# Kernel optimization log

Hardware: AMD Instinct MI355X
Metric: run time of the kernel (lower is better)

## Reference

```python
import jax, jax.numpy as jnp
import numpy as np

N_NODES = 50000

def _graph_conv(x, src, dst, W, b, n):
    # DGL GraphConv, norm='both': D_dst^{-1/2} * sum_edges(D_src^{-1/2} * (x W)) + b
    xw = x @ W  # [N, out]
    ones = jnp.ones(src.shape, jnp.float32)
    deg_out = jnp.maximum(jax.ops.segment_sum(ones, src, num_segments=n), 1.0)
    deg_in = jnp.maximum(jax.ops.segment_sum(ones, dst, num_segments=n), 1.0)
    norm_src = deg_out ** -0.5
    norm_dst = deg_in ** -0.5
    msg = xw[src] * norm_src[src][:, None]          # [E, out] gather
    agg = jax.ops.segment_sum(msg, dst, num_segments=n)  # [N, out] scatter-add
    return agg * norm_dst[:, None] + b


def _rgcn_layer(x, src, dst, W, b, n):
    # HeteroGraphConv with aggregate='sum' over relations
    out = _graph_conv(x, src[0], dst[0], W[0], b[0], n)
    for r in range(1, src.shape[0]):
        out = out + _graph_conv(x, src[r], dst[r], W[r], b[r], n)
    return out


def setup_inputs() -> dict:
    key = jax.random.key(0)
    ks = jax.random.split(key, 9)
    R, E = 3, 200000
    din, dhid, dout = 128, 128, 64
    x = jax.random.normal(ks[0], (N_NODES, din), jnp.float32)
    src = jax.random.randint(ks[1], (R, E), 0, N_NODES, jnp.int32)
    dst = jax.random.randint(ks[2], (R, E), 0, N_NODES, jnp.int32)
    neg_src = jax.random.randint(ks[3], (E,), 0, N_NODES, jnp.int32)
    neg_dst = jax.random.randint(ks[4], (E,), 0, N_NODES, jnp.int32)
    W1 = jax.random.normal(ks[5], (R, din, dhid), jnp.float32) / np.sqrt(din)
    b1 = jnp.zeros((R, dhid), jnp.float32)
    W2 = jax.random.normal(ks[6], (R, dhid, dout), jnp.float32) / np.sqrt(dhid)
    b2 = jnp.zeros((R, dout), jnp.float32)
    return {"x": x, "src": src, "dst": dst, "neg_src": neg_src,
            "neg_dst": neg_dst, "W1": W1, "b1": b1, "W2": W2, "b2": b2}


def reference(x, src, dst, neg_src, neg_dst, W1, b1, W2, b2):
    n = x.shape[0]
    h = jax.nn.relu(_rgcn_layer(x, src, dst, W1, b1, n))
    h = _rgcn_layer(h, src, dst, W2, b2, n)  # [N, out]
    # HeteroDotProductPredictor on etype = relation 0 (u_dot_v -> [E, 1])
    pos = jnp.sum(h[src[0]] * h[dst[0]], axis=-1, keepdims=True)
    neg = jnp.sum(h[neg_src] * h[neg_dst], axis=-1, keepdims=True)
    return pos, neg
```

## Files before the change

### kernel.cpp

```cpp
#include <hip/hip_runtime.h>

#define N_NODES 50000
#define E_EDGES 200000
#define R_REL 3
#define D_IN 128
#define D_HID 128
#define D_OUT 64
#define N_SCAN (R_REL * N_NODES)
#define BCAP 16
#define OVCAP 4096

typedef __attribute__((ext_vector_type(8))) short bf16x8;
typedef __attribute__((ext_vector_type(4))) float f32x4;

__device__ inline unsigned short f2bf(float v) {
    union { float f; unsigned int u; } x; x.f = v;
    unsigned int r = x.u + 0x7fffu + ((x.u >> 16) & 1u);
    return (unsigned short)(r >> 16);
}
__device__ inline float bf2f(unsigned short h) {
    union { unsigned int u; float f; } x; x.u = ((unsigned int)h) << 16; return x.f;
}
__device__ inline float bf_lo(unsigned int p) {
    union { unsigned int u; float f; } x; x.u = p << 16; return x.f;
}
__device__ inline float bf_hi(unsigned int p) {
    union { unsigned int u; float f; } x; x.u = p & 0xffff0000u; return x.f;
}

__global__ __launch_bounds__(256) void k_zero_i32(int* __restrict__ p, int n) {
    int i = blockIdx.x * 256 + threadIdx.x;
    if (i < n) p[i] = 0;
}

__global__ __launch_bounds__(256) void k_count_prep(const int* __restrict__ src,
                                                    const int* __restrict__ dst,
                                                    const float* __restrict__ x,
                                                    const float* __restrict__ W1,
                                                    const float* __restrict__ W2,
                                                    const float* __restrict__ b1,
                                                    int* __restrict__ deg_out,
                                                    int* __restrict__ cnt_in,
                                                    int* __restrict__ ov_cnt,
                                                    uint2* __restrict__ ovlist,
                                                    int* __restrict__ bucket,
                                                    unsigned int* __restrict__ xb,
                                                    unsigned short* __restrict__ w1t_h,
                                                    unsigned short* __restrict__ w1t_l,
                                                    unsigned short* __restrict__ w2t_h,
                                                    unsigned short* __restrict__ w2t_l,
                                                    float* __restrict__ bsum) {
    int i = blockIdx.x * 256 + threadIdx.x;
    if (i < 400000) {
#pragma unroll
        for (int k = 0; k < 4; k++) {
            int q = i * 4 + k;
            float4 v = ((const float4*)x)[q];
            uint2 u;
            u.x = ((unsigned int)f2bf(v.y) << 16) | f2bf(v.x);
            u.y = ((unsigned int)f2bf(v.w) << 16) | f2bf(v.z);
            ((uint2*)xb)[q] = u;
        }
    }
    if (i < R_REL * D_IN * D_HID) {
        int r = i >> 14;
        int kk = (i >> 7) & 127;
        int c = i & 127;
        float v = W1[i];
        unsigned short h = f2bf(v);
        unsigned short l = f2bf(v - bf2f(h));
        int o = r * 16384 + c * 128 + kk;
        w1t_h[o] = h;
        w1t_l[o] = l;
    }
    if (i < R_REL * D_HID * D_OUT) {
        int r = i >> 13;
        int kk = (i >> 6) & 127;
        int cl = i & 63;
        float v = W2[i];
        unsigned short h = f2bf(v);
        unsigned short l = f2bf(v - bf2f(h));
        int o = (r * 64 + cl) * 128 + kk;
        w2t_h[o] = h;
        w2t_l[o] = l;
    }
    if (i < 128) bsum[i] = b1[i] + b1[128 + i] + b1[256 + i];
    if (i < R_REL * E_EDGES) {
        int r = i / E_EDGES;
        int s = src[i];
        int d = dst[i];
        atomicAdd(&deg_out[r * N_NODES + s], 1);
        int bin = r * N_NODES + d;
        int pos = atomicAdd(&cnt_in[bin], 1);
        if (pos < BCAP) {
            bucket[bin * BCAP + pos] = s;
        } else {
            int oi = atomicAdd(ov_cnt, 1);
            if (oi < OVCAP) {
                uint2 e;
                e.x = (unsigned int)bin;
                e.y = (unsigned int)s;
                ovlist[oi] = e;
            }
        }
    }
}

__global__ __launch_bounds__(256) void k_rednorm(const int* __restrict__ deg_out,
                                                 const int* __restrict__ cnt_in,
                                                 float* __restrict__ norm_out,
                                                 float* __restrict__ norm_in) {
    int b = blockIdx.x * 256 + threadIdx.x;
    if (b >= N_SCAN) return;
    int o = deg_out[b];
    int d = cnt_in[b];
    norm_out[b] = rsqrtf((float)(o > 1 ? o : 1));
    norm_in[b] = rsqrtf((float)(d > 1 ? d : 1));
}

__global__ __launch_bounds__(256) void k_agg128(const int* __restrict__ cnt_r,
                                                const int* __restrict__ bucket_r,
                                                const float* __restrict__ nout_r,
                                                const float* __restrict__ nin_r,
                                                const int* __restrict__ ov_cnt,
                                                const uint2* __restrict__ ovlist,
                                                int rbase,
                                                const unsigned int* __restrict__ xb,
                                                float* __restrict__ agg) {
    int w = (blockIdx.x * 256 + threadIdx.x) >> 6;
    if (w >= N_NODES) return;
    int lane = threadIdx.x & 63;
    const unsigned int* tab = xb + lane;
    int n = cnt_r[w];
    int nn = n < BCAP ? n : BCAP;
    float ax = 0.f, ay = 0.f;
    int j = 0;
    for (; j + 4 <= nn; j += 4) {
        uint4 s4 = *(const uint4*)&bucket_r[w * BCAP + j];
        float c0 = nout_r[s4.x], c1 = nout_r[s4.y];
        float c2 = nout_r[s4.z], c3 = nout_r[s4.w];
        unsigned int p0 = tab[s4.x * 64], p1 = tab[s4.y * 64];
        unsigned int p2 = tab[s4.z * 64], p3 = tab[s4.w * 64];
        ax += c0 * bf_lo(p0); ay += c0 * bf_hi(p0);
        ax += c1 * bf_lo(p1); ay += c1 * bf_hi(p1);
        ax += c2 * bf_lo(p2); ay += c2 * bf_hi(p2);
        ax += c3 * bf_lo(p3); ay += c3 * bf_hi(p3);
    }
    for (; j < nn; j++) {
        unsigned int s = (unsigned int)bucket_r[w * BCAP + j];
        float c = nout_r[s];
        unsigned int p = tab[s * 64];
        ax += c * bf_lo(p);
        ay += c * bf_hi(p);
    }
    int oc = *ov_cnt;
    if (oc > 0) {
        if (oc > OVCAP) oc = OVCAP;
        for (int k = 0; k < oc; k++) {
            uint2 e = ovlist[k];
            if ((int)e.x == rbase + w) {
                float c = nout_r[e.y];
                unsigned int p = tab[e.y * 64];
                ax += c * bf_lo(p);
                ay += c * bf_hi(p);
            }
        }
    }
    float ni = nin_r[w];
    float2 o;
    o.x = ax * ni;
    o.y = ay * ni;
    *(float2*)&agg[w * 128 + lane * 2] = o;
}

template <int MODE>
__global__ __launch_bounds__(256) void k_mm1(const float* __restrict__ A,
                                             const unsigned short* __restrict__ wt_h,
                                             const unsigned short* __restrict__ wt_l,
                                             const float* __restrict__ bsum,
                                             float* __restrict__ h1f,
                                             unsigned short* __restrict__ h1h,
                                             unsigned short* __restrict__ h1l,
                                             int M) {
    __shared__ short sAh[2048], sAl[2048];
    __shared__ short sWh[4096], sWl[4096];
    int t = threadIdx.x;
    int row0 = blockIdx.x * 64;
    int wid = t >> 6;
    int lane = t & 63;
    int lr = lane & 15;
    int lkg = lane >> 4;
    int wr = (wid & 1) * 32;
    int wc = (wid >> 1) * 64;

    f32x4 acc[2][4];
#pragma unroll
    for (int i = 0; i < 2; i++)
#pragma unroll
        for (int j = 0; j < 4; j++) acc[i][j] = (f32x4)(0.f);

    int arow = t >> 2;
    int akg = t & 3;

    for (int k0 = 0; k0 < 128; k0 += 32) {
        {
            int gr = row0 + arow;
            float v[8];
            if (gr < M) {
                float4 p0 = *(const float4*)&A[gr * 128 + k0 + akg * 8];
                float4 p1 = *(const float4*)&A[gr * 128 + k0 + akg * 8 + 4];
                v[0] = p0.x; v[1] = p0.y; v[2] = p0.z; v[3] = p0.w;
                v[4] = p1.x; v[5] = p1.y; v[6] = p1.z; v[7] = p1.w;
            } else {
#pragma unroll
                for (int e = 0; e < 8; e++) v[e] = 0.f;
            }
            short hh[8], ll[8];
#pragma unroll
            for (int e = 0; e < 8; e++) {
                unsigned short h = f2bf(v[e]);
                hh[e] = (short)h;
                ll[e] = (short)f2bf(v[e] - bf2f(h));
            }
            int cidx = akg * 64 + arow;
            *(bf16x8*)&sAh[cidx * 8] = *(bf16x8*)hh;
            *(bf16x8*)&sAl[cidx * 8] = *(bf16x8*)ll;
        }
#pragma unroll
        for (int itr = 0; itr < 2; itr++) {
            int cc = t + itr * 256;
            int col = cc >> 2;
            int kg = cc & 3;
            int go = col * 128 + k0 + kg * 8;
            int cidx = kg * 128 + col;
            *(bf16x8*)&sWh[cidx * 8] = *(const bf16x8*)&wt_h[go];
            *(bf16x8*)&sWl[cidx * 8] = *(const bf16x8*)&wt_l[go];
        }
        __syncthreads();
        bf16x8 ah[2], al[2], bh[4], bl[4];
#pragma unroll
        for (int i = 0; i < 2; i++) {
            int cidx = lkg * 64 + wr + i * 16 + lr;
            ah[i] = *(const bf16x8*)&sAh[cidx * 8];
            al[i] = *(const bf16x8*)&sAl[cidx * 8];
        }
#pragma unroll
        for (int j = 0; j < 4; j++) {
            int cidx = lkg * 128 + wc + j * 16 + lr;
            bh[j] = *(const bf16x8*)&sWh[cidx * 8];
            bl[j] = *(const bf16x8*)&sWl[cidx * 8];
        }
#pragma unroll
        for (int i = 0; i < 2; i++)
#pragma unroll
            for (int j = 0; j < 4; j++) {
                acc[i][j] = __builtin_amdgcn_mfma_f32_16x16x32_bf16(ah[i], bh[j], acc[i][j], 0, 0, 0);
                acc[i][j] = __builtin_amdgcn_mfma_f32_16x16x32_bf16(ah[i], bl[j], acc[i][j], 0, 0, 0);
                acc[i][j] = __builtin_amdgcn_mfma_f32_16x16x32_bf16(al[i], bh[j], acc[i][j], 0, 0, 0);
            }
        __syncthreads();
    }
#pragma unroll
    for (int i = 0; i < 2; i++)
#pragma unroll
        for (int q = 0; q < 4; q++) {
            int gr = row0 + wr + i * 16 + lkg * 4 + q;
            if (gr >= M) continue;
#pragma unroll
            for (int j = 0; j < 4; j++) {
                int gc = wc + j * 16 + lr;
                float v = acc[i][j][q];
                if (MODE == 0) {
                    h1f[gr * 128 + gc] = v + bsum[gc];
                } else if (MODE == 1) {
                    h1f[gr * 128 + gc] += v;
                } else {
                    float u = fmaxf(h1f[gr * 128 + gc] + v, 0.f);
                    unsigned short h = f2bf(u);
                    h1h[gr * 128 + gc] = h;
                    h1l[gr * 128 + gc] = f2bf(u - bf2f(h));
                }
            }
        }
}

__global__ __launch_bounds__(256) void k_mm2(const unsigned short* __restrict__ h1h,
                                             const unsigned short* __restrict__ h1l,
                                             const unsigned short* __restrict__ wt_h,
                                             const unsigned short* __restrict__ wt_l,
                                             const float* __restrict__ norm_out,
                                             unsigned short* __restrict__ xwb2, int M) {
    __shared__ short sAh[2048], sAl[2048];
    __shared__ short sWh[6144], sWl[6144];
    int t = threadIdx.x;
    int row0 = blockIdx.x * 64;
    int wid = t >> 6;
    int lane = t & 63;
    int lr = lane & 15;
    int lkg = lane >> 4;
    int wr = (wid & 1) * 32;
    int wc = (wid >> 1) * 96;

    f32x4 acc[2][6];
#pragma unroll
    for (int i = 0; i < 2; i++)
#pragma unroll
        for (int j = 0; j < 6; j++) acc[i][j] = (f32x4)(0.f);

    int arow = t >> 2;
    int akg = t & 3;

    for (int k0 = 0; k0 < 128; k0 += 32) {
        {
            int gr = row0 + arow;
            int cidx = akg * 64 + arow;
            if (gr < M) {
                int go = gr * 128 + k0 + akg * 8;
                *(bf16x8*)&sAh[cidx * 8] = *(const bf16x8*)&h1h[go];
                *(bf16x8*)&sAl[cidx * 8] = *(const bf16x8*)&h1l[go];
            } else {
                *(bf16x8*)&sAh[cidx * 8] = (bf16x8)(short)0;
                *(bf16x8*)&sAl[cidx * 8] = (bf16x8)(short)0;
            }
        }
#pragma unroll
        for (int itr = 0; itr < 3; itr++) {
            int cc = t + itr * 256;
            int col = cc >> 2;
            int kg = cc & 3;
            int go = col * 128 + k0 + kg * 8;
            int cidx = kg * 192 + col;
            *(bf16x8*)&sWh[cidx * 8] = *(const bf16x8*)&wt_h[go];
            *(bf16x8*)&sWl[cidx * 8] = *(const bf16x8*)&wt_l[go];
        }
        __syncthreads();
        bf16x8 ah[2], al[2];
#pragma unroll
        for (int i = 0; i < 2; i++) {
            int cidx = lkg * 64 + wr + i * 16 + lr;
            ah[i] = *(const bf16x8*)&sAh[cidx * 8];
            al[i] = *(const bf16x8*)&sAl[cidx * 8];
        }
#pragma unroll
        for (int j = 0; j < 6; j++) {
            int cidx = lkg * 192 + wc + j * 16 + lr;
            bf16x8 bh = *(const bf16x8*)&sWh[cidx * 8];
            bf16x8 bl = *(const bf16x8*)&sWl[cidx * 8];
#pragma unroll
            for (int i = 0; i < 2; i++) {
                acc[i][j] = __builtin_amdgcn_mfma_f32_16x16x32_bf16(ah[i], bh, acc[i][j], 0, 0, 0);
                acc[i][j] = __builtin_amdgcn_mfma_f32_16x16x32_bf16(ah[i], bl, acc[i][j], 0, 0, 0);
                acc[i][j] = __builtin_amdgcn_mfma_f32_16x16x32_bf16(al[i], bh, acc[i][j], 0, 0, 0);
            }
        }
        __syncthreads();
    }
#pragma unroll
    for (int i = 0; i < 2; i++)
#pragma unroll
        for (int q = 0; q < 4; q++) {
            int gr = row0 + wr + i * 16 + lkg * 4 + q;
            if (gr >= M) continue;
#pragma unroll
            for (int j = 0; j < 6; j++) {
                int gc = wc + j * 16 + lr;
                float sc = norm_out[(gc >> 6) * N_NODES + gr];
                xwb2[gr * 192 + gc] = f2bf(acc[i][j][q] * sc);
            }
        }
}

__global__ __launch_bounds__(256) void k_agg64f(const int* __restrict__ cnt_in,
                                                const int* __restrict__ bucket,
                                                const float* __restrict__ norm_in,
                                                const int* __restrict__ ov_cnt,
                                                const uint2* __restrict__ ovlist,
                                                const unsigned short* __restrict__ xwb,
                                                const float* __restrict__ b2,
                                                unsigned short* __restrict__ h2b) {
    int w = (blockIdx.x * 256 + threadIdx.x) >> 6;
    if (w >= N_NODES) return;
    int lane = threadIdx.x & 63;
    float acc = b2[lane] + b2[64 + lane] + b2[128 + lane];
    int oc = *ov_cnt;
    if (oc > OVCAP) oc = OVCAP;
#pragma unroll
    for (int r = 0; r < R_REL; r++) {
        const unsigned short* tab = xwb + r * 64 + lane;
        int bin = r * N_NODES + w;
        int n = cnt_in[bin];
        int nn = n < BCAP ? n : BCAP;
        float a = 0.f;
        int j = 0;
        for (; j + 4 <= nn; j += 4) {
            uint4 s4 = *(const uint4*)&bucket[bin * BCAP + j];
            float v0 = bf2f(tab[s4.x * 192]);
            float v1 = bf2f(tab[s4.y * 192]);
            float v2 = bf2f(tab[s4.z * 192]);
            float v3 = bf2f(tab[s4.w * 192]);
            a += v0 + v1 + v2 + v3;
        }
        for (; j < nn; j++) {
            unsigned int s = (unsigned int)bucket[bin * BCAP + j];
            a += bf2f(tab[s * 192]);
        }
        if (oc > 0) {
            for (int k = 0; k < oc; k++) {
                uint2 e = ovlist[k];
                if ((int)e.x == bin) a += bf2f(tab[e.y * 192]);
            }
        }
        acc += norm_in[bin] * a;
    }
    h2b[w * 64 + lane] = f2bf(acc);
}

__global__ __launch_bounds__(256) void k_predict(const int* __restrict__ sa,
                                                 const int* __restrict__ sb,
                                                 const int* __restrict__ na,
                                                 const int* __restrict__ nb,
                                                 const unsigned short* __restrict__ h2b,
                                                 float* __restrict__ out) {
    int tid = blockIdx.x * 256 + threadIdx.x;
    int p = tid >> 4;
    if (p >= 2 * E_EDGES) return;
    int lane = tid & 15;
    int ia, ib;
    if (p < E_EDGES) { ia = sa[p]; ib = sb[p]; }
    else             { ia = na[p - E_EDGES]; ib = nb[p - E_EDGES]; }
    uint2 ua = *(const uint2*)&h2b[ia * 64 + lane * 4];
    uint2 ub = *(const uint2*)&h2b[ib * 64 + lane * 4];
    float d = bf_lo(ua.x) * bf_lo(ub.x) + bf_hi(ua.x) * bf_hi(ub.x)
            + bf_lo(ua.y) * bf_lo(ub.y) + bf_hi(ua.y) * bf_hi(ub.y);
    d += __shfl_xor(d, 1);
    d += __shfl_xor(d, 2);
    d += __shfl_xor(d, 4);
    d += __shfl_xor(d, 8);
    if (lane == 0) out[p] = d;
}


extern "C" void kernel_launch(void* const* d_in, const int* in_sizes, int n_in,
                              void* d_out, int out_size, void* d_ws, size_t ws_size,
                              hipStream_t stream) {
    (void)in_sizes; (void)n_in; (void)out_size; (void)ws_size;
    const float* x       = (const float*)d_in[0];
    const int*   src     = (const int*)d_in[1];
    const int*   dst     = (const int*)d_in[2];
    const int*   neg_src = (const int*)d_in[3];
    const int*   neg_dst = (const int*)d_in[4];
    const float* W1      = (const float*)d_in[5];
    const float* b1      = (const float*)d_in[6];
    const float* W2      = (const float*)d_in[7];
    const float* b2      = (const float*)d_in[8];
    float* out = (float*)d_out;
    float* ws  = (float*)d_ws;

    float* norm_out = ws;
    float* norm_in  = ws + N_SCAN;
    int*   deg_out  = (int*)(ws + 300000);
    int*   cnt_in   = (int*)(ws + 450000);
    int*   ov_cnt   = (int*)(ws + 600000);
    uint2* ovlist   = (uint2*)(ws + 600016);
    int*   bucket   = (int*)(ws + 608208);
    unsigned short* w1t_h = (unsigned short*)(ws + 3008208);
    unsigned short* w1t_l = (unsigned short*)(ws + 3032784);
    unsigned short* w2t_h = (unsigned short*)(ws + 3057360);
    unsigned short* w2t_l = (unsigned short*)(ws + 3069648);
    float* bsum     = ws + 3081936;
    float* agg      = ws + 3082064;
    unsigned short* xwb2 = (unsigned short*)(ws + 3082064);
    float* h1f      = ws + 9482064;
    unsigned short* h2b  = (unsigned short*)(ws + 9482064);
    unsigned short* h1h  = (unsigned short*)(ws + 15882064);
    unsigned short* h1l  = (unsigned short*)(ws + 19082064);
    unsigned int*   xb   = (unsigned int*)(ws + 19082064);

    const int NB_CP   = (R_REL * E_EDGES + 255) / 256;
    const int NB_WAVE = (N_NODES * 64 + 255) / 256;
    const int NB_MM   = (N_NODES + 63) / 64;

    k_zero_i32<<<(300016 + 255) / 256, 256, 0, stream>>>(deg_out, 300016);
    k_count_prep<<<NB_CP, 256, 0, stream>>>(src, dst, x, W1, W2, b1,
                                            deg_out, cnt_in, ov_cnt, ovlist, bucket,
                                            xb, w1t_h, w1t_l, w2t_h, w2t_l, bsum);
    k_rednorm<<<(N_SCAN + 255) / 256, 256, 0, stream>>>(deg_out, cnt_in, norm_out, norm_in);

    for (int r = 0; r < R_REL; r++) {
        k_agg128<<<NB_WAVE, 256, 0, stream>>>(cnt_in + r * N_NODES,
                                              bucket + r * N_NODES * BCAP,
                                              norm_out + r * N_NODES,
                                              norm_in + r * N_NODES,
                                              ov_cnt, ovlist, r * N_NODES, xb, agg);
        if (r == 0)
            k_mm1<0><<<NB_MM, 256, 0, stream>>>(agg, w1t_h, w1t_l, bsum, h1f, h1h, h1l, N_NODES);
        else if (r == 1)
            k_mm1<1><<<NB_MM, 256, 0, stream>>>(agg, w1t_h + 16384, w1t_l + 16384, bsum, h1f, h1h, h1l, N_NODES);
        else
            k_mm1<2><<<NB_MM, 256, 0, stream>>>(agg, w1t_h + 32768, w1t_l + 32768, bsum, h1f, h1h, h1l, N_NODES);
    }

    k_mm2<<<NB_MM, 256, 0, stream>>>(h1h, h1l, w2t_h, w2t_l, norm_out, xwb2, N_NODES);
    k_agg64f<<<NB_WAVE, 256, 0, stream>>>(cnt_in, bucket, norm_in, ov_cnt, ovlist,
                                          xwb2, b2, h2b);

    k_predict<<<(2 * E_EDGES * 16 + 255) / 256, 256, 0, stream>>>(
        src, dst, neg_src, neg_dst, h2b, out);
}
```

Before: 272.2 us.

## Batch layer-1 aggregation across relations, store bf16, fuse into one K=384 GEMM

The three per-relation aggregate+GEMM launch pairs become one aggregation kernel over a 2D grid (node, relation) that writes normalized aggregates as bf16. A single GEMM then runs K=384 across the concatenated relation aggregates with bias and ReLU in the epilogue, so the fp32 h1 read-modify-write passes and the A-side hi/lo split are gone. This drops one of the three MFMAs per tile. The count_prep grid is also interleaved so edge-counting blocks and conversion blocks mix, and bucket indices are loaded as four uint4 into an unrolled predicated loop. The cost is lower precision: the aggregated activations lose their low bf16 part.

```diff
diff --git a/kernel.cpp b/kernel.cpp
--- a/kernel.cpp
+++ b/kernel.cpp
@@ -9,6 +9,8 @@
 #define N_SCAN (R_REL * N_NODES)
 #define BCAP 16
 #define OVCAP 4096
+#define NBE 2344
+#define NBP 1563
 
 typedef __attribute__((ext_vector_type(8))) short bf16x8;
 typedef __attribute__((ext_vector_type(4))) float f32x4;
@@ -50,42 +52,13 @@
                                                     unsigned short* __restrict__ w2t_h,
                                                     unsigned short* __restrict__ w2t_l,
                                                     float* __restrict__ bsum) {
-    int i = blockIdx.x * 256 + threadIdx.x;
-    if (i < 400000) {
-#pragma unroll
-        for (int k = 0; k < 4; k++) {
-            int q = i * 4 + k;
-            float4 v = ((const float4*)x)[q];
-            uint2 u;
-            u.x = ((unsigned int)f2bf(v.y) << 16) | f2bf(v.x);
-            u.y = ((unsigned int)f2bf(v.w) << 16) | f2bf(v.z);
-            ((uint2*)xb)[q] = u;
-        }
-    }
-    if (i < R_REL * D_IN * D_HID) {
-        int r = i >> 14;
-        int kk = (i >> 7) & 127;
-        int c = i & 127;
-        float v = W1[i];
-        unsigned short h = f2bf(v);
-        unsigned short l = f2bf(v - bf2f(h));
-        int o = r * 16384 + c * 128 + kk;
-        w1t_h[o] = h;
-        w1t_l[o] = l;
-    }
-    if (i < R_REL * D_HID * D_OUT) {
-        int r = i >> 13;
-        int kk = (i >> 6) & 127;
-        int cl = i & 63;
-        float v = W2[i];
-        unsigned short h = f2bf(v);
-        unsigned short l = f2bf(v - bf2f(h));
-        int o = (r * 64 + cl) * 128 + kk;
-        w2t_h[o] = h;
-        w2t_l[o] = l;
-    }
-    if (i < 128) bsum[i] = b1[i] + b1[128 + i] + b1[256 + i];
-    if (i < R_REL * E_EDGES) {
+    int g = blockIdx.x / 5;
+    int m = blockIdx.x % 5;
+    int t = threadIdx.x;
+    if (m < 3) {
+        int eb = g * 3 + m;
+        int i = eb * 256 + t;
+        if (i >= R_REL * E_EDGES) return;
         int r = i / E_EDGES;
         int s = src[i];
         int d = dst[i];
@@ -103,6 +76,43 @@
                 ovlist[oi] = e;
             }
         }
+    } else {
+        int pb = g * 2 + (m - 3);
+        int i = pb * 256 + t;
+        if (i < 400000) {
+#pragma unroll
+            for (int k = 0; k < 4; k++) {
+                int q = i * 4 + k;
+                float4 v = ((const float4*)x)[q];
+                uint2 u;
+                u.x = ((unsigned int)f2bf(v.y) << 16) | f2bf(v.x);
+                u.y = ((unsigned int)f2bf(v.w) << 16) | f2bf(v.z);
+                ((uint2*)xb)[q] = u;
+            }
+        }
+        if (i < R_REL * D_IN * D_HID) {
+            int r = i >> 14;
+            int kk = (i >> 7) & 127;
+            int c = i & 127;
+            float v = W1[i];
+            unsigned short h = f2bf(v);
+            unsigned short l = f2bf(v - bf2f(h));
+            int o = r * 16384 + c * 128 + kk;
+            w1t_h[o] = h;
+            w1t_l[o] = l;
+        }
+        if (i < R_REL * D_HID * D_OUT) {
+            int r = i >> 13;
+            int kk = (i >> 6) & 127;
+            int cl = i & 63;
+            float v = W2[i];
+            unsigned short h = f2bf(v);
+            unsigned short l = f2bf(v - bf2f(h));
+            int o = (r * 64 + cl) * 128 + kk;
+            w2t_h[o] = h;
+            w2t_l[o] = l;
+        }
+        if (i < 128) bsum[i] = b1[i] + b1[128 + i] + b1[256 + i];
     }
 }
 
@@ -118,71 +128,64 @@
     norm_in[b] = rsqrtf((float)(d > 1 ? d : 1));
 }
 
-__global__ __launch_bounds__(256) void k_agg128(const int* __restrict__ cnt_r,
-                                                const int* __restrict__ bucket_r,
-                                                const float* __restrict__ nout_r,
-                                                const float* __restrict__ nin_r,
+__global__ __launch_bounds__(256) void k_aggall(const int* __restrict__ cnt_in,
+                                                const int* __restrict__ bucket,
+                                                const float* __restrict__ norm_out,
+                                                const float* __restrict__ norm_in,
                                                 const int* __restrict__ ov_cnt,
                                                 const uint2* __restrict__ ovlist,
-                                                int rbase,
                                                 const unsigned int* __restrict__ xb,
-                                                float* __restrict__ agg) {
+                                                unsigned int* __restrict__ aggh) {
     int w = (blockIdx.x * 256 + threadIdx.x) >> 6;
     if (w >= N_NODES) return;
+    int r = blockIdx.y;
     int lane = threadIdx.x & 63;
     const unsigned int* tab = xb + lane;
-    int n = cnt_r[w];
+    const float* nout = norm_out + r * N_NODES;
+    int bin = r * N_NODES + w;
+    int n = cnt_in[bin];
+    const uint4* bp = (const uint4*)(bucket + bin * BCAP);
+    uint4 q0 = bp[0], q1 = bp[1], q2 = bp[2], q3 = bp[3];
+    unsigned int sl[16] = {q0.x, q0.y, q0.z, q0.w, q1.x, q1.y, q1.z, q1.w,
+                           q2.x, q2.y, q2.z, q2.w, q3.x, q3.y, q3.z, q3.w};
     int nn = n < BCAP ? n : BCAP;
     float ax = 0.f, ay = 0.f;
-    int j = 0;
-    for (; j + 4 <= nn; j += 4) {
-        uint4 s4 = *(const uint4*)&bucket_r[w * BCAP + j];
-        float c0 = nout_r[s4.x], c1 = nout_r[s4.y];
-        float c2 = nout_r[s4.z], c3 = nout_r[s4.w];
-        unsigned int p0 = tab[s4.x * 64], p1 = tab[s4.y * 64];
-        unsigned int p2 = tab[s4.z * 64], p3 = tab[s4.w * 64];
-        ax += c0 * bf_lo(p0); ay += c0 * bf_hi(p0);
-        ax += c1 * bf_lo(p1); ay += c1 * bf_hi(p1);
-        ax += c2 * bf_lo(p2); ay += c2 * bf_hi(p2);
-        ax += c3 * bf_lo(p3); ay += c3 * bf_hi(p3);
-    }
-    for (; j < nn; j++) {
-        unsigned int s = (unsigned int)bucket_r[w * BCAP + j];
-        float c = nout_r[s];
-        unsigned int p = tab[s * 64];
-        ax += c * bf_lo(p);
-        ay += c * bf_hi(p);
+#pragma unroll
+    for (int j = 0; j < BCAP; j++) {
+        if (j < nn) {
+            unsigned int s = sl[j];
+            float c = nout[s];
+            unsigned int p = tab[s * 64];
+            ax += c * bf_lo(p);
+            ay += c * bf_hi(p);
+        }
     }
     int oc = *ov_cnt;
     if (oc > 0) {
         if (oc > OVCAP) oc = OVCAP;
         for (int k = 0; k < oc; k++) {
             uint2 e = ovlist[k];
-            if ((int)e.x == rbase + w) {
-                float c = nout_r[e.y];
+            if ((int)e.x == bin) {
+                float c = nout[e.y];
                 unsigned int p = tab[e.y * 64];
                 ax += c * bf_lo(p);
                 ay += c * bf_hi(p);
             }
         }
     }
-    float ni = nin_r[w];
-    float2 o;
-    o.x = ax * ni;
-    o.y = ay * ni;
-    *(float2*)&agg[w * 128 + lane * 2] = o;
-}
-
-template <int MODE>
-__global__ __launch_bounds__(256) void k_mm1(const float* __restrict__ A,
-                                             const unsigned short* __restrict__ wt_h,
-                                             const unsigned short* __restrict__ wt_l,
-                                             const float* __restrict__ bsum,
-                                             float* __restrict__ h1f,
-                                             unsigned short* __restrict__ h1h,
-                                             unsigned short* __restrict__ h1l,
-                                             int M) {
-    __shared__ short sAh[2048], sAl[2048];
+    float ni = norm_in[bin];
+    unsigned int o = ((unsigned int)f2bf(ay * ni) << 16) | f2bf(ax * ni);
+    aggh[bin * 64 + lane] = o;
+}
+
+__global__ __launch_bounds__(256) void k_mm1f(const unsigned short* __restrict__ aggh,
+                                              const unsigned short* __restrict__ wt_h,
+                                              const unsigned short* __restrict__ wt_l,
+                                              const float* __restrict__ bsum,
+                                              unsigned short* __restrict__ h1h,
+                                              unsigned short* __restrict__ h1l,
+                                              int M) {
+    __shared__ short sA[2048];
     __shared__ short sWh[4096], sWl[4096];
     int t = threadIdx.x;
     int row0 = blockIdx.x * 64;
@@ -202,47 +205,34 @@
     int arow = t >> 2;
     int akg = t & 3;
 
-    for (int k0 = 0; k0 < 128; k0 += 32) {
+    for (int k0 = 0; k0 < 384; k0 += 32) {
+        int rr = k0 >> 7;
+        int kk = k0 & 127;
         {
             int gr = row0 + arow;
-            float v[8];
-            if (gr < M) {
-                float4 p0 = *(const float4*)&A[gr * 128 + k0 + akg * 8];
-                float4 p1 = *(const float4*)&A[gr * 128 + k0 + akg * 8 + 4];
-                v[0] = p0.x; v[1] = p0.y; v[2] = p0.z; v[3] = p0.w;
-                v[4] = p1.x; v[5] = p1.y; v[6] = p1.z; v[7] = p1.w;
-            } else {
-#pragma unroll
-                for (int e = 0; e < 8; e++) v[e] = 0.f;
-            }
-            short hh[8], ll[8];
-#pragma unroll
-            for (int e = 0; e < 8; e++) {
-                unsigned short h = f2bf(v[e]);
-                hh[e] = (short)h;
-                ll[e] = (short)f2bf(v[e] - bf2f(h));
-            }
             int cidx = akg * 64 + arow;
-            *(bf16x8*)&sAh[cidx * 8] = *(bf16x8*)hh;
-            *(bf16x8*)&sAl[cidx * 8] = *(bf16x8*)ll;
+            if (gr < M)
+                *(bf16x8*)&sA[cidx * 8] =
+                    *(const bf16x8*)&aggh[(rr * N_NODES + gr) * 128 + kk + akg * 8];
+            else
+                *(bf16x8*)&sA[cidx * 8] = (bf16x8)(short)0;
         }
 #pragma unroll
         for (int itr = 0; itr < 2; itr++) {
             int cc = t + itr * 256;
             int col = cc >> 2;
             int kg = cc & 3;
-            int go = col * 128 + k0 + kg * 8;
+            int go = rr * 16384 + col * 128 + kk + kg * 8;
             int cidx = kg * 128 + col;
             *(bf16x8*)&sWh[cidx * 8] = *(const bf16x8*)&wt_h[go];
             *(bf16x8*)&sWl[cidx * 8] = *(const bf16x8*)&wt_l[go];
         }
         __syncthreads();
-        bf16x8 ah[2], al[2], bh[4], bl[4];
+        bf16x8 a[2], bh[4], bl[4];
 #pragma unroll
         for (int i = 0; i < 2; i++) {
             int cidx = lkg * 64 + wr + i * 16 + lr;
-            ah[i] = *(const bf16x8*)&sAh[cidx * 8];
-            al[i] = *(const bf16x8*)&sAl[cidx * 8];
+            a[i] = *(const bf16x8*)&sA[cidx * 8];
         }
 #pragma unroll
         for (int j = 0; j < 4; j++) {
@@ -254,9 +244,8 @@
         for (int i = 0; i < 2; i++)
 #pragma unroll
             for (int j = 0; j < 4; j++) {
-                acc[i][j] = __builtin_amdgcn_mfma_f32_16x16x32_bf16(ah[i], bh[j], acc[i][j], 0, 0, 0);
-                acc[i][j] = __builtin_amdgcn_mfma_f32_16x16x32_bf16(ah[i], bl[j], acc[i][j], 0, 0, 0);
-                acc[i][j] = __builtin_amdgcn_mfma_f32_16x16x32_bf16(al[i], bh[j], acc[i][j], 0, 0, 0);
+                acc[i][j] = __builtin_amdgcn_mfma_f32_16x16x32_bf16(a[i], bh[j], acc[i][j], 0, 0, 0);
+                acc[i][j] = __builtin_amdgcn_mfma_f32_16x16x32_bf16(a[i], bl[j], acc[i][j], 0, 0, 0);
             }
         __syncthreads();
     }
@@ -269,17 +258,10 @@
 #pragma unroll
             for (int j = 0; j < 4; j++) {
                 int gc = wc + j * 16 + lr;
-                float v = acc[i][j][q];
-                if (MODE == 0) {
-                    h1f[gr * 128 + gc] = v + bsum[gc];
-                } else if (MODE == 1) {
-                    h1f[gr * 128 + gc] += v;
-                } else {
-                    float u = fmaxf(h1f[gr * 128 + gc] + v, 0.f);
-                    unsigned short h = f2bf(u);
-                    h1h[gr * 128 + gc] = h;
-                    h1l[gr * 128 + gc] = f2bf(u - bf2f(h));
-                }
+                float u = fmaxf(acc[i][j][q] + bsum[gc], 0.f);
+                unsigned short h = f2bf(u);
+                h1h[gr * 128 + gc] = h;
+                h1l[gr * 128 + gc] = f2bf(u - bf2f(h));
             }
         }
 }
@@ -389,20 +371,15 @@
         const unsigned short* tab = xwb + r * 64 + lane;
         int bin = r * N_NODES + w;
         int n = cnt_in[bin];
+        const uint4* bp = (const uint4*)(bucket + bin * BCAP);
+        uint4 q0 = bp[0], q1 = bp[1], q2 = bp[2], q3 = bp[3];
+        unsigned int sl[16] = {q0.x, q0.y, q0.z, q0.w, q1.x, q1.y, q1.z, q1.w,
+                               q2.x, q2.y, q2.z, q2.w, q3.x, q3.y, q3.z, q3.w};
         int nn = n < BCAP ? n : BCAP;
         float a = 0.f;
-        int j = 0;
-        for (; j + 4 <= nn; j += 4) {
-            uint4 s4 = *(const uint4*)&bucket[bin * BCAP + j];
-            float v0 = bf2f(tab[s4.x * 192]);
-            float v1 = bf2f(tab[s4.y * 192]);
-            float v2 = bf2f(tab[s4.z * 192]);
-            float v3 = bf2f(tab[s4.w * 192]);
-            a += v0 + v1 + v2 + v3;
-        }
-        for (; j < nn; j++) {
-            unsigned int s = (unsigned int)bucket[bin * BCAP + j];
-            a += bf2f(tab[s * 192]);
+#pragma unroll
+        for (int j = 0; j < BCAP; j++) {
+            if (j < nn) a += bf2f(tab[sl[j] * 192]);
         }
         if (oc > 0) {
             for (int k = 0; k < oc; k++) {
@@ -468,37 +445,27 @@
     unsigned short* w2t_h = (unsigned short*)(ws + 3057360);
     unsigned short* w2t_l = (unsigned short*)(ws + 3069648);
     float* bsum     = ws + 3081936;
-    float* agg      = ws + 3082064;
+    unsigned int*   aggh = (unsigned int*)(ws + 3082064);
     unsigned short* xwb2 = (unsigned short*)(ws + 3082064);
-    float* h1f      = ws + 9482064;
-    unsigned short* h2b  = (unsigned short*)(ws + 9482064);
-    unsigned short* h1h  = (unsigned short*)(ws + 15882064);
-    unsigned short* h1l  = (unsigned short*)(ws + 19082064);
-    unsigned int*   xb   = (unsigned int*)(ws + 19082064);
-
-    const int NB_CP   = (R_REL * E_EDGES + 255) / 256;
+    unsigned short* h1h  = (unsigned short*)(ws + 12682064);
+    unsigned short* h2b  = (unsigned short*)(ws + 12682064);
+    unsigned short* h1l  = (unsigned short*)(ws + 15882064);
+    unsigned int*   xb   = (unsigned int*)(ws + 15882064);
+
     const int NB_WAVE = (N_NODES * 64 + 255) / 256;
     const int NB_MM   = (N_NODES + 63) / 64;
 
     k_zero_i32<<<(300016 + 255) / 256, 256, 0, stream>>>(deg_out, 300016);
-    k_count_prep<<<NB_CP, 256, 0, stream>>>(src, dst, x, W1, W2, b1,
-                                            deg_out, cnt_in, ov_cnt, ovlist, bucket,
-                                            xb, w1t_h, w1t_l, w2t_h, w2t_l, bsum);
+    k_count_prep<<<782 * 5, 256, 0, stream>>>(src, dst, x, W1, W2, b1,
+                                              deg_out, cnt_in, ov_cnt, ovlist, bucket,
+                                              xb, w1t_h, w1t_l, w2t_h, w2t_l, bsum);
     k_rednorm<<<(N_SCAN + 255) / 256, 256, 0, stream>>>(deg_out, cnt_in, norm_out, norm_in);
 
-    for (int r = 0; r < R_REL; r++) {
-        k_agg128<<<NB_WAVE, 256, 0, stream>>>(cnt_in + r * N_NODES,
-                                              bucket + r * N_NODES * BCAP,
-                                              norm_out + r * N_NODES,
-                                              norm_in + r * N_NODES,
-                                              ov_cnt, ovlist, r * N_NODES, xb, agg);
-        if (r == 0)
-            k_mm1<0><<<NB_MM, 256, 0, stream>>>(agg, w1t_h, w1t_l, bsum, h1f, h1h, h1l, N_NODES);
-        else if (r == 1)
-            k_mm1<1><<<NB_MM, 256, 0, stream>>>(agg, w1t_h + 16384, w1t_l + 16384, bsum, h1f, h1h, h1l, N_NODES);
-        else
-            k_mm1<2><<<NB_MM, 256, 0, stream>>>(agg, w1t_h + 32768, w1t_l + 32768, bsum, h1f, h1h, h1l, N_NODES);
-    }
+    dim3 gagg(NB_WAVE, R_REL);
+    k_aggall<<<gagg, 256, 0, stream>>>(cnt_in, bucket, norm_out, norm_in,
+                                       ov_cnt, ovlist, xb, aggh);
+    k_mm1f<<<NB_MM, 256, 0, stream>>>((const unsigned short*)aggh, w1t_h, w1t_l, bsum,
+                                      h1h, h1l, N_NODES);
 
     k_mm2<<<NB_MM, 256, 0, stream>>>(h1h, h1l, w2t_h, w2t_l, norm_out, xwb2, N_NODES);
     k_agg64f<<<NB_WAVE, 256, 0, stream>>>(cnt_in, bucket, norm_in, ov_cnt, ovlist,
```

Measured after the change: 259.5 us. -4.7%, faster.
